# Performance work log

Measured on AMD Instinct MI355X. Metric: run time of the kernel, lower is better.

The kernel has to match this reference:

```python
import jax, jax.numpy as jnp
import numpy as np

B, H1, W1, C = 16, 32, 32, 256
H2, W2, C2 = 16, 16, 512
H3, W3, C3 = 8, 8, 1024
N1, N2, N3 = H1 * W1, H2 * W2, H3 * W3


def resize_bilinear_legacy(x, out_size):
    """Legacy tf.image.resize_images BILINEAR (align_corners=False,
    half_pixel_centers=False): src = dst * in/out. x: [B, H, W]."""
    def lerp_axis(a, in_size, axis):
        src = jnp.arange(out_size, dtype=jnp.float32) * (in_size / out_size)
        lo = jnp.floor(src).astype(jnp.int32)
        hi = jnp.minimum(lo + 1, in_size - 1)
        fr = (src - lo.astype(jnp.float32))
        shape = [1, 1, 1]
        shape[axis] = out_size
        fr = fr.reshape(shape)
        a_lo = jnp.take(a, lo, axis=axis)
        a_hi = jnp.take(a, hi, axis=axis)
        return a_lo * (1.0 - fr) + a_hi * fr

    x = lerp_axis(x, x.shape[1], axis=1)
    x = lerp_axis(x, x.shape[2], axis=2)
    return x


def setup_inputs() -> dict:
    key = jax.random.key(0)
    ks = jax.random.split(key, 10)
    s = lambda c: 1.0 / np.sqrt(c)
    return {
        "f1": jax.random.normal(ks[0], (B, H1, W1, C), jnp.float32),
        "f2": jax.random.normal(ks[1], (B, H2, W2, C2), jnp.float32),
        "f3": jax.random.normal(ks[2], (B, H3, W3, C3), jnp.float32),
        "w1": jax.random.normal(ks[3], (C, C), jnp.float32) * s(C),
        "b1": jnp.zeros((C,), jnp.float32),
        "w2": jax.random.normal(ks[4], (C2, C), jnp.float32) * s(C2),
        "b2": jnp.zeros((C,), jnp.float32),
        "w3": jax.random.normal(ks[5], (C3, C), jnp.float32) * s(C3),
        "b3": jnp.zeros((C,), jnp.float32),
        # Keras 'uniform' init: U(-0.05, 0.05), shape (1,)
        "a1": jax.random.uniform(ks[6], (1,), jnp.float32, -0.05, 0.05),
        "a2": jax.random.uniform(ks[7], (1,), jnp.float32, -0.05, 0.05),
        "a3": jax.random.uniform(ks[8], (1,), jnp.float32, -0.05, 0.05),
    }


def reference(f1, f2, f3, w1, b1, w2, b2, w3, b3, a1, a2, a3):
    # 1x1 conv projections to C channels
    p1 = jnp.einsum("bhwc,cd->bhwd", f1, w1) + b1          # [B,H1,W1,C]
    p2 = jnp.einsum("bhwc,cd->bhwd", f2, w2) + b2          # [B,H2,W2,C]
    p3 = jnp.einsum("bhwc,cd->bhwd", f3, w3) + b3          # [B,H3,W3,C]

    x1 = p1.reshape(B, N1, C)
    x2 = p2.reshape(B, N2, C)
    x3 = p3.reshape(B, N3, C)

    att1 = jnp.einsum("bnc,bmc->bnm", x1, x1)              # [B,N1,N1]
    att2 = jnp.einsum("bnc,bmc->bnm", x2, x2)              # [B,N2,N2]
    att3 = jnp.einsum("bnc,bmc->bnm", x3, x3)              # [B,N3,N3]

    att2 = resize_bilinear_legacy(att2, N1)                # [B,N1,N1]
    att3 = resize_bilinear_legacy(att3, N1)                # [B,N1,N1]

    att = jax.nn.sigmoid(a1[0] * att1 + a2[0] * att2 + a3[0] * att3)

    out = jnp.einsum("bnm,bmc->bnc", att, x1)              # [B,N1,C]
    return p1 + out.reshape(B, H1, W1, C)
```

## Files before the change

### kernel.cpp

```cpp
#include <hip/hip_runtime.h>

typedef unsigned short ushort_t;
typedef short s16x8 __attribute__((ext_vector_type(8)));
typedef float f32x4 __attribute__((ext_vector_type(4)));

#define MFMA16(a, b, c) __builtin_amdgcn_mfma_f32_16x16x32_bf16((a), (b), (c), 0, 0, 0)

#define BATCH 16
#define N1 1024
#define C1 256
#define N2 256
#define N3 64
#define PB3 64
#define PB2 256
#define PB1 256
#define TSTRIDE 72

static __device__ __forceinline__ ushort_t f2b(float f) {
    unsigned int u = __builtin_bit_cast(unsigned int, f);
    unsigned int r = (u + 0x7fffu + ((u >> 16) & 1u)) >> 16;
    return (ushort_t)r;
}
static __device__ __forceinline__ float b2f(ushort_t b) {
    unsigned int u = ((unsigned int)b) << 16;
    return __builtin_bit_cast(float, u);
}

static __device__ __forceinline__ s16x8 cvt8(const float* p) {
    f32x4 lo = *reinterpret_cast<const f32x4*>(p);
    f32x4 hi = *reinterpret_cast<const f32x4*>(p + 4);
    s16x8 r;
#pragma unroll
    for (int i = 0; i < 4; ++i) {
        r[i]     = (short)f2b(lo[i]);
        r[i + 4] = (short)f2b(hi[i]);
    }
    return r;
}

__global__ void k_wt(const float* __restrict__ w1, const float* __restrict__ w2,
                     const float* __restrict__ w3,
                     ushort_t* __restrict__ w1t, ushort_t* __restrict__ w2t,
                     ushort_t* __restrict__ w3t) {
    int i = blockIdx.x * 256 + threadIdx.x;
    if (i < 65536) {
        int d = i >> 8, k = i & 255;
        w1t[i] = f2b(w1[k * 256 + d]);
    } else if (i < 65536 + 131072) {
        int j = i - 65536;
        int d = j >> 9, k = j & 511;
        w2t[j] = f2b(w2[k * 256 + d]);
    } else if (i < 65536 + 131072 + 262144) {
        int j = i - 65536 - 131072;
        int d = j >> 10, k = j & 1023;
        w3t[j] = f2b(w3[k * 256 + d]);
    }
}

__global__ __launch_bounds__(256) void k_proj(
    const float* __restrict__ f1, const float* __restrict__ f2,
    const float* __restrict__ f3,
    const ushort_t* __restrict__ w1t, const ushort_t* __restrict__ w2t,
    const ushort_t* __restrict__ w3t,
    const float* __restrict__ b1, const float* __restrict__ b2,
    const float* __restrict__ b3,
    ushort_t* __restrict__ x1b, ushort_t* __restrict__ x1t,
    ushort_t* __restrict__ x2b, ushort_t* __restrict__ x3b)
{
    __shared__ ushort_t sT[256 * TSTRIDE];

    int bid = blockIdx.x;
    int w = threadIdx.x >> 6, l = threadIdx.x & 63;
    int lr = l & 15, lk = (l >> 4) * 8;

    if (bid < PB3 + PB2) {
        const float* A; const ushort_t* wt; const float* bias; ushort_t* xb; int K, tile;
        if (bid < PB3) { A = f3; wt = w3t; bias = b3; xb = x3b; K = 1024; tile = bid; }
        else           { A = f2; wt = w2t; bias = b2; xb = x2b; K = 512;  tile = bid - PB3; }
        int rowBase = tile * 16;

        const float* arow = A + (size_t)(rowBase + lr) * K + lk;
        f32x4 acc[4] = {};
        for (int kk = 0; kk < K; kk += 32) {
            s16x8 af = cvt8(arow + kk);
#pragma unroll
            for (int t = 0; t < 4; ++t) {
                const ushort_t* bp = wt + (size_t)(w * 64 + t * 16 + lr) * K + kk + lk;
                acc[t] = MFMA16(af, *reinterpret_cast<const s16x8*>(bp), acc[t]);
            }
        }
        int r0 = rowBase + (l >> 4) * 4;
#pragma unroll
        for (int t = 0; t < 4; ++t) {
            int c = w * 64 + t * 16 + lr;
            float bs = bias[c];
#pragma unroll
            for (int j = 0; j < 4; ++j) {
                float v = acc[t][j] + bs;
                xb[(size_t)(r0 + j) * 256 + c] = f2b(v);
            }
        }
    } else {
        int tile = bid - PB3 - PB2;
        int rowBase = tile * 64;
        const float* arow = f1 + (size_t)(rowBase + w * 16 + lr) * 256 + lk;

        f32x4 acc[16] = {};
        for (int kk = 0; kk < 256; kk += 32) {
            s16x8 af = cvt8(arow + kk);
#pragma unroll
            for (int t = 0; t < 16; ++t) {
                const ushort_t* bp = w1t + (size_t)(t * 16 + lr) * 256 + kk + lk;
                acc[t] = MFMA16(af, *reinterpret_cast<const s16x8*>(bp), acc[t]);
            }
        }
        int rl0 = w * 16 + (l >> 4) * 4;
        int r0 = rowBase + rl0;
#pragma unroll
        for (int t = 0; t < 16; ++t) {
            int c = t * 16 + lr;
            float bs = b1[c];
#pragma unroll
            for (int j = 0; j < 4; ++j) {
                float v = acc[t][j] + bs;
                ushort_t bits = f2b(v);
                x1b[(size_t)(r0 + j) * 256 + c] = bits;
                sT[c * TSTRIDE + rl0 + j] = bits;
            }
        }
        __syncthreads();
        int b = rowBase >> 10;
        int mBase = rowBase & 1023;
        int q = threadIdx.x & 3;
#pragma unroll
        for (int it = 0; it < 4; ++it) {
            int c = it * 64 + (threadIdx.x >> 2);
            const uint4* src = reinterpret_cast<const uint4*>(&sT[c * TSTRIDE + q * 16]);
            uint4* dst = reinterpret_cast<uint4*>(&x1t[((size_t)b * 256 + c) * 1024 + mBase + q * 16]);
            dst[0] = src[0];
            dst[1] = src[1];
        }
    }
}

__global__ __launch_bounds__(256) void k_xxt(
    const ushort_t* __restrict__ x2b, const ushort_t* __restrict__ x3b,
    float* __restrict__ att2, float* __restrict__ att3)
{
    int bid = blockIdx.x;
    const ushort_t* x; float* att; int n, b, bx, by;
    if (bid < 16) { x = x3b; att = att3; n = 64; b = bid; bx = 0; by = 0; }
    else {
        int j = bid - 16;
        x = x2b; att = att2; n = 256;
        b = j >> 4; bx = (j & 15) & 3; by = (j & 15) >> 2;
    }
    int w = threadIdx.x >> 6, l = threadIdx.x & 63;
    int lr = l & 15, lk = (l >> 4) * 8;
    int rowBase = bx * 64 + (w >> 1) * 32;
    int colBase = by * 64 + (w & 1) * 32;
    const ushort_t* xb = x + (size_t)b * n * 256;

    f32x4 acc[2][2] = {};
    for (int kk = 0; kk < 256; kk += 32) {
        s16x8 a[2], bb[2];
#pragma unroll
        for (int i = 0; i < 2; ++i)
            a[i] = *reinterpret_cast<const s16x8*>(xb + (size_t)(rowBase + i * 16 + lr) * 256 + kk + lk);
#pragma unroll
        for (int j = 0; j < 2; ++j)
            bb[j] = *reinterpret_cast<const s16x8*>(xb + (size_t)(colBase + j * 16 + lr) * 256 + kk + lk);
#pragma unroll
        for (int i = 0; i < 2; ++i)
#pragma unroll
            for (int j = 0; j < 2; ++j)
                acc[i][j] = MFMA16(a[i], bb[j], acc[i][j]);
    }
    float* ab = att + (size_t)b * n * n;
#pragma unroll
    for (int i = 0; i < 2; ++i)
#pragma unroll
        for (int j = 0; j < 2; ++j)
#pragma unroll
            for (int q = 0; q < 4; ++q) {
                int r = rowBase + i * 16 + (l >> 4) * 4 + q;
                int c = colBase + j * 16 + lr;
                ab[(size_t)r * n + c] = acc[i][j][q];
            }
}

__global__ __launch_bounds__(256) void k_att(
    const ushort_t* __restrict__ x1b, const float* __restrict__ att2,
    const float* __restrict__ att3,
    const float* __restrict__ a1p, const float* __restrict__ a2p, const float* __restrict__ a3p,
    ushort_t* __restrict__ att)
{
    int b = blockIdx.z;
    int w = threadIdx.x >> 6, l = threadIdx.x & 63;
    int lr = l & 15, lk = (l >> 4) * 8;
    int rowBase = blockIdx.x * 128 + (w >> 1) * 64;
    int colBase = blockIdx.y * 128 + (w & 1) * 64;
    const ushort_t* xb = x1b + (size_t)b * N1 * C1;

    f32x4 acc[4][4] = {};
    for (int kk = 0; kk < 256; kk += 32) {
        s16x8 a[4], bb[4];
#pragma unroll
        for (int i = 0; i < 4; ++i)
            a[i] = *reinterpret_cast<const s16x8*>(xb + (size_t)(rowBase + i * 16 + lr) * 256 + kk + lk);
#pragma unroll
        for (int j = 0; j < 4; ++j)
            bb[j] = *reinterpret_cast<const s16x8*>(xb + (size_t)(colBase + j * 16 + lr) * 256 + kk + lk);
#pragma unroll
        for (int i = 0; i < 4; ++i)
#pragma unroll
            for (int j = 0; j < 4; ++j)
                acc[i][j] = MFMA16(a[i], bb[j], acc[i][j]);
    }

    float a1 = *a1p, a2 = *a2p, a3 = *a3p;
    const float* A2 = att2 + (size_t)b * N2 * N2;
    const float* A3 = att3 + (size_t)b * N3 * N3;
    ushort_t* ab = att + (size_t)b * N1 * N1;

#pragma unroll
    for (int i = 0; i < 4; ++i)
#pragma unroll
        for (int j = 0; j < 4; ++j)
#pragma unroll
            for (int q = 0; q < 4; ++q) {
                int nn = rowBase + i * 16 + (l >> 4) * 4 + q;
                int mm = colBase + j * 16 + lr;
                int r2l = nn >> 2, c2l = mm >> 2;
                int r2h = min(r2l + 1, N2 - 1), c2h = min(c2l + 1, N2 - 1);
                float fr2 = (float)(nn & 3) * 0.25f, fc2 = (float)(mm & 3) * 0.25f;
                float v2 =
                    (1.f - fr2) * ((1.f - fc2) * A2[r2l * N2 + c2l] + fc2 * A2[r2l * N2 + c2h]) +
                    fr2 * ((1.f - fc2) * A2[r2h * N2 + c2l] + fc2 * A2[r2h * N2 + c2h]);
                int r3l = nn >> 4, c3l = mm >> 4;
                int r3h = min(r3l + 1, N3 - 1), c3h = min(c3l + 1, N3 - 1);
                float fr3 = (float)(nn & 15) * 0.0625f, fc3 = (float)(mm & 15) * 0.0625f;
                float v3 =
                    (1.f - fr3) * ((1.f - fc3) * A3[r3l * N3 + c3l] + fc3 * A3[r3l * N3 + c3h]) +
                    fr3 * ((1.f - fc3) * A3[r3h * N3 + c3l] + fc3 * A3[r3h * N3 + c3h]);
                float s = a1 * acc[i][j][q] + a2 * v2 + a3 * v3;
                float sig = 1.f / (1.f + __expf(-s));
                ab[(size_t)nn * N1 + mm] = f2b(sig);
            }
}

__global__ __launch_bounds__(256) void k_pv(
    const ushort_t* __restrict__ att, const ushort_t* __restrict__ x1t,
    const ushort_t* __restrict__ x1b, float* __restrict__ out)
{
    int b = blockIdx.z;
    int w = threadIdx.x >> 6, l = threadIdx.x & 63;
    int lr = l & 15, lk = (l >> 4) * 8;
    int rowBase = blockIdx.x * 128 + (w >> 1) * 64;
    int colBase = blockIdx.y * 128 + (w & 1) * 64;
    const ushort_t* ab = att + (size_t)b * N1 * N1;
    const ushort_t* xt = x1t + (size_t)b * C1 * N1;

    f32x4 acc[4][4] = {};
    for (int kk = 0; kk < 1024; kk += 32) {
        s16x8 a[4], bb[4];
#pragma unroll
        for (int i = 0; i < 4; ++i)
            a[i] = *reinterpret_cast<const s16x8*>(ab + (size_t)(rowBase + i * 16 + lr) * N1 + kk + lk);
#pragma unroll
        for (int j = 0; j < 4; ++j)
            bb[j] = *reinterpret_cast<const s16x8*>(xt + (size_t)(colBase + j * 16 + lr) * N1 + kk + lk);
#pragma unroll
        for (int i = 0; i < 4; ++i)
#pragma unroll
            for (int j = 0; j < 4; ++j)
                acc[i][j] = MFMA16(a[i], bb[j], acc[i][j]);
    }
#pragma unroll
    for (int i = 0; i < 4; ++i)
#pragma unroll
        for (int j = 0; j < 4; ++j)
#pragma unroll
            for (int q = 0; q < 4; ++q) {
                int r = rowBase + i * 16 + (l >> 4) * 4 + q;
                int c = colBase + j * 16 + lr;
                size_t idx = ((size_t)b * N1 + r) * C1 + c;
                out[idx] = b2f(x1b[idx]) + acc[i][j][q];
            }
}

extern "C" void kernel_launch(void* const* d_in, const int* in_sizes, int n_in,
                              void* d_out, int out_size, void* d_ws, size_t ws_size,
                              hipStream_t stream) {
    const float* f1 = (const float*)d_in[0];
    const float* f2 = (const float*)d_in[1];
    const float* f3 = (const float*)d_in[2];
    const float* w1 = (const float*)d_in[3];
    const float* b1 = (const float*)d_in[4];
    const float* w2 = (const float*)d_in[5];
    const float* b2 = (const float*)d_in[6];
    const float* w3 = (const float*)d_in[7];
    const float* b3 = (const float*)d_in[8];
    const float* a1 = (const float*)d_in[9];
    const float* a2 = (const float*)d_in[10];
    const float* a3 = (const float*)d_in[11];

    char* ws = (char*)d_ws;
    size_t off = 0;
    auto alloc = [&](size_t bytes) -> void* {
        void* p = ws + off;
        off += (bytes + 255) & ~(size_t)255;
        return p;
    };
    ushort_t* w1t = (ushort_t*)alloc((size_t)256 * 256 * 2);
    ushort_t* w2t = (ushort_t*)alloc((size_t)256 * 512 * 2);
    ushort_t* w3t = (ushort_t*)alloc((size_t)256 * 1024 * 2);
    ushort_t* x1b = (ushort_t*)alloc((size_t)BATCH * N1 * C1 * 2);
    ushort_t* x1t = (ushort_t*)alloc((size_t)BATCH * N1 * C1 * 2);
    ushort_t* x2b = (ushort_t*)alloc((size_t)BATCH * N2 * C1 * 2);
    ushort_t* x3b = (ushort_t*)alloc((size_t)BATCH * N3 * C1 * 2);
    float*    att2 = (float*)alloc((size_t)BATCH * N2 * N2 * 4);
    float*    att3 = (float*)alloc((size_t)BATCH * N3 * N3 * 4);
    ushort_t* attb = (ushort_t*)alloc((size_t)BATCH * N1 * N1 * 2);

    k_wt<<<(65536 + 131072 + 262144 + 255) / 256, 256, 0, stream>>>(w1, w2, w3, w1t, w2t, w3t);

    k_proj<<<PB3 + PB2 + PB1, 256, 0, stream>>>(f1, f2, f3, w1t, w2t, w3t,
                                                b1, b2, b3, x1b, x1t, x2b, x3b);

    k_xxt<<<16 + 256, 256, 0, stream>>>(x2b, x3b, att2, att3);

    k_att<<<dim3(N1 / 128, N1 / 128, BATCH), 256, 0, stream>>>(x1b, att2, att3, a1, a2, a3, attb);

    k_pv<<<dim3(N1 / 128, C1 / 128, BATCH), 256, 0, stream>>>(attb, x1t, x1b, (float*)d_out);
}
```

Baseline: 247.0 us.

## Fuse attention score, sigmoid and PV into flash-style kernel without materialized matrix

Merges the attention-score kernel and the P·V kernel into one streaming kernel. Each wave keeps 16 query rows in registers, computes 16x32 score tiles, applies bilinear-resized att2/att3 and the sigmoid, reshuffles the tile into A-operand layout with lane shuffles, and accumulates against V. This avoids writing and re-reading the 16x1024x1024 bf16 attention matrix. The trade-off is a grid of only 256 blocks with no LDS reuse, so every wave reloads keys and V from cache. The projection of f1 is also retiled to 32-row blocks with a smaller transpose buffer, and a few loops get unroll pragmas.

```diff
diff --git a/kernel.cpp b/kernel.cpp
--- a/kernel.cpp
+++ b/kernel.cpp
@@ -13,8 +13,8 @@
 #define N3 64
 #define PB3 64
 #define PB2 256
-#define PB1 256
-#define TSTRIDE 72
+#define PB1 512
+#define TST 40
 
 static __device__ __forceinline__ ushort_t f2b(float f) {
     unsigned int u = __builtin_bit_cast(unsigned int, f);
@@ -57,6 +57,35 @@
     }
 }
 
+template <int K>
+static __device__ __forceinline__ void proj16(
+    const float* __restrict__ A, const ushort_t* __restrict__ wt,
+    const float* __restrict__ bias, ushort_t* __restrict__ xb,
+    int tile, int w, int lr, int lk)
+{
+    int rowBase = tile * 16;
+    const float* arow = A + (size_t)(rowBase + lr) * K + lk;
+    f32x4 acc[4] = {};
+#pragma unroll 4
+    for (int kk = 0; kk < K; kk += 32) {
+        s16x8 af = cvt8(arow + kk);
+#pragma unroll
+        for (int t = 0; t < 4; ++t) {
+            const ushort_t* bp = wt + (size_t)(w * 64 + t * 16 + lr) * K + kk + lk;
+            acc[t] = MFMA16(af, *reinterpret_cast<const s16x8*>(bp), acc[t]);
+        }
+    }
+    int r0 = rowBase + (lk >> 3) * 4;
+#pragma unroll
+    for (int t = 0; t < 4; ++t) {
+        int c = w * 64 + t * 16 + lr;
+        float bs = bias[c];
+#pragma unroll
+        for (int j = 0; j < 4; ++j)
+            xb[(size_t)(r0 + j) * 256 + c] = f2b(acc[t][j] + bs);
+    }
+}
+
 __global__ __launch_bounds__(256) void k_proj(
     const float* __restrict__ f1, const float* __restrict__ f2,
     const float* __restrict__ f3,
@@ -67,79 +96,52 @@
     ushort_t* __restrict__ x1b, ushort_t* __restrict__ x1t,
     ushort_t* __restrict__ x2b, ushort_t* __restrict__ x3b)
 {
-    __shared__ ushort_t sT[256 * TSTRIDE];
+    __shared__ ushort_t sT[256 * TST];
 
     int bid = blockIdx.x;
     int w = threadIdx.x >> 6, l = threadIdx.x & 63;
-    int lr = l & 15, lk = (l >> 4) * 8;
-
-    if (bid < PB3 + PB2) {
-        const float* A; const ushort_t* wt; const float* bias; ushort_t* xb; int K, tile;
-        if (bid < PB3) { A = f3; wt = w3t; bias = b3; xb = x3b; K = 1024; tile = bid; }
-        else           { A = f2; wt = w2t; bias = b2; xb = x2b; K = 512;  tile = bid - PB3; }
-        int rowBase = tile * 16;
-
-        const float* arow = A + (size_t)(rowBase + lr) * K + lk;
-        f32x4 acc[4] = {};
-        for (int kk = 0; kk < K; kk += 32) {
+    int lr = l & 15, g = l >> 4, lk = g * 8;
+
+    if (bid < PB3) {
+        proj16<1024>(f3, w3t, b3, x3b, bid, w, lr, lk);
+    } else if (bid < PB3 + PB2) {
+        proj16<512>(f2, w2t, b2, x2b, bid - PB3, w, lr, lk);
+    } else {
+        int tile = bid - PB3 - PB2;
+        int rowBase = tile * 32;
+        int rowHalf = w & 1, colHalf = w >> 1;
+        const float* arow = f1 + (size_t)(rowBase + rowHalf * 16 + lr) * 256 + lk;
+
+        f32x4 acc[8] = {};
+#pragma unroll 2
+        for (int kk = 0; kk < 256; kk += 32) {
             s16x8 af = cvt8(arow + kk);
 #pragma unroll
-            for (int t = 0; t < 4; ++t) {
-                const ushort_t* bp = wt + (size_t)(w * 64 + t * 16 + lr) * K + kk + lk;
+            for (int t = 0; t < 8; ++t) {
+                const ushort_t* bp = w1t + (size_t)(colHalf * 128 + t * 16 + lr) * 256 + kk + lk;
                 acc[t] = MFMA16(af, *reinterpret_cast<const s16x8*>(bp), acc[t]);
             }
         }
-        int r0 = rowBase + (l >> 4) * 4;
-#pragma unroll
-        for (int t = 0; t < 4; ++t) {
-            int c = w * 64 + t * 16 + lr;
-            float bs = bias[c];
-#pragma unroll
-            for (int j = 0; j < 4; ++j) {
-                float v = acc[t][j] + bs;
-                xb[(size_t)(r0 + j) * 256 + c] = f2b(v);
-            }
-        }
-    } else {
-        int tile = bid - PB3 - PB2;
-        int rowBase = tile * 64;
-        const float* arow = f1 + (size_t)(rowBase + w * 16 + lr) * 256 + lk;
-
-        f32x4 acc[16] = {};
-        for (int kk = 0; kk < 256; kk += 32) {
-            s16x8 af = cvt8(arow + kk);
-#pragma unroll
-            for (int t = 0; t < 16; ++t) {
-                const ushort_t* bp = w1t + (size_t)(t * 16 + lr) * 256 + kk + lk;
-                acc[t] = MFMA16(af, *reinterpret_cast<const s16x8*>(bp), acc[t]);
-            }
-        }
-        int rl0 = w * 16 + (l >> 4) * 4;
-        int r0 = rowBase + rl0;
-#pragma unroll
-        for (int t = 0; t < 16; ++t) {
-            int c = t * 16 + lr;
+        int rl0 = rowHalf * 16 + g * 4;
+#pragma unroll
+        for (int t = 0; t < 8; ++t) {
+            int c = colHalf * 128 + t * 16 + lr;
             float bs = b1[c];
 #pragma unroll
             for (int j = 0; j < 4; ++j) {
                 float v = acc[t][j] + bs;
                 ushort_t bits = f2b(v);
-                x1b[(size_t)(r0 + j) * 256 + c] = bits;
-                sT[c * TSTRIDE + rl0 + j] = bits;
+                x1b[(size_t)(rowBase + rl0 + j) * 256 + c] = bits;
+                sT[c * TST + rl0 + j] = bits;
             }
         }
         __syncthreads();
-        int b = rowBase >> 10;
-        int mBase = rowBase & 1023;
-        int q = threadIdx.x & 3;
-#pragma unroll
-        for (int it = 0; it < 4; ++it) {
-            int c = it * 64 + (threadIdx.x >> 2);
-            const uint4* src = reinterpret_cast<const uint4*>(&sT[c * TSTRIDE + q * 16]);
-            uint4* dst = reinterpret_cast<uint4*>(&x1t[((size_t)b * 256 + c) * 1024 + mBase + q * 16]);
-            dst[0] = src[0];
-            dst[1] = src[1];
-        }
+        int b = rowBase >> 10, mBase = rowBase & 1023;
+        int c = threadIdx.x;
+        const uint4* src = reinterpret_cast<const uint4*>(&sT[c * TST]);
+        uint4* dst = reinterpret_cast<uint4*>(&x1t[(((size_t)b * 256 + c) << 10) + mBase]);
+#pragma unroll
+        for (int q = 0; q < 4; ++q) dst[q] = src[q];
     }
 }
 
@@ -162,6 +164,7 @@
     const ushort_t* xb = x + (size_t)b * n * 256;
 
     f32x4 acc[2][2] = {};
+#pragma unroll 2
     for (int kk = 0; kk < 256; kk += 32) {
         s16x8 a[2], bb[2];
 #pragma unroll
@@ -189,104 +192,98 @@
             }
 }
 
-__global__ __launch_bounds__(256) void k_att(
-    const ushort_t* __restrict__ x1b, const float* __restrict__ att2,
-    const float* __restrict__ att3,
-    const float* __restrict__ a1p, const float* __restrict__ a2p, const float* __restrict__ a3p,
-    ushort_t* __restrict__ att)
+__global__ __launch_bounds__(256) void k_attpv(
+    const ushort_t* __restrict__ x1b, const ushort_t* __restrict__ x1t,
+    const float* __restrict__ att2, const float* __restrict__ att3,
+    const float* __restrict__ a1p, const float* __restrict__ a2p,
+    const float* __restrict__ a3p, float* __restrict__ out)
 {
-    int b = blockIdx.z;
+    int b = blockIdx.y;
     int w = threadIdx.x >> 6, l = threadIdx.x & 63;
-    int lr = l & 15, lk = (l >> 4) * 8;
-    int rowBase = blockIdx.x * 128 + (w >> 1) * 64;
-    int colBase = blockIdx.y * 128 + (w & 1) * 64;
-    const ushort_t* xb = x1b + (size_t)b * N1 * C1;
-
-    f32x4 acc[4][4] = {};
-    for (int kk = 0; kk < 256; kk += 32) {
-        s16x8 a[4], bb[4];
-#pragma unroll
-        for (int i = 0; i < 4; ++i)
-            a[i] = *reinterpret_cast<const s16x8*>(xb + (size_t)(rowBase + i * 16 + lr) * 256 + kk + lk);
-#pragma unroll
-        for (int j = 0; j < 4; ++j)
-            bb[j] = *reinterpret_cast<const s16x8*>(xb + (size_t)(colBase + j * 16 + lr) * 256 + kk + lk);
-#pragma unroll
-        for (int i = 0; i < 4; ++i)
-#pragma unroll
-            for (int j = 0; j < 4; ++j)
-                acc[i][j] = MFMA16(a[i], bb[j], acc[i][j]);
-    }
-
-    float a1 = *a1p, a2 = *a2p, a3 = *a3p;
+    int idx = l & 15, g = l >> 4;
+    int rowBase = blockIdx.x * 64 + w * 16;
+    const ushort_t* X = x1b + (size_t)b * N1 * C1;
+    const ushort_t* V = x1t + (size_t)b * C1 * N1;
+
+    s16x8 rf[8];
+    const ushort_t* rowp = X + (size_t)(rowBase + idx) * 256 + g * 8;
+#pragma unroll
+    for (int ks = 0; ks < 8; ++ks) rf[ks] = *reinterpret_cast<const s16x8*>(rowp + ks * 32);
+
+    int nn = rowBase + idx;
     const float* A2 = att2 + (size_t)b * N2 * N2;
     const float* A3 = att3 + (size_t)b * N3 * N3;
-    ushort_t* ab = att + (size_t)b * N1 * N1;
-
-#pragma unroll
-    for (int i = 0; i < 4; ++i)
-#pragma unroll
-        for (int j = 0; j < 4; ++j)
-#pragma unroll
-            for (int q = 0; q < 4; ++q) {
-                int nn = rowBase + i * 16 + (l >> 4) * 4 + q;
-                int mm = colBase + j * 16 + lr;
-                int r2l = nn >> 2, c2l = mm >> 2;
-                int r2h = min(r2l + 1, N2 - 1), c2h = min(c2l + 1, N2 - 1);
-                float fr2 = (float)(nn & 3) * 0.25f, fc2 = (float)(mm & 3) * 0.25f;
-                float v2 =
-                    (1.f - fr2) * ((1.f - fc2) * A2[r2l * N2 + c2l] + fc2 * A2[r2l * N2 + c2h]) +
-                    fr2 * ((1.f - fc2) * A2[r2h * N2 + c2l] + fc2 * A2[r2h * N2 + c2h]);
-                int r3l = nn >> 4, c3l = mm >> 4;
-                int r3h = min(r3l + 1, N3 - 1), c3h = min(c3l + 1, N3 - 1);
-                float fr3 = (float)(nn & 15) * 0.0625f, fc3 = (float)(mm & 15) * 0.0625f;
-                float v3 =
-                    (1.f - fr3) * ((1.f - fc3) * A3[r3l * N3 + c3l] + fc3 * A3[r3l * N3 + c3h]) +
-                    fr3 * ((1.f - fc3) * A3[r3h * N3 + c3l] + fc3 * A3[r3h * N3 + c3h]);
-                float s = a1 * acc[i][j][q] + a2 * v2 + a3 * v3;
-                float sig = 1.f / (1.f + __expf(-s));
-                ab[(size_t)nn * N1 + mm] = f2b(sig);
-            }
-}
-
-__global__ __launch_bounds__(256) void k_pv(
-    const ushort_t* __restrict__ att, const ushort_t* __restrict__ x1t,
-    const ushort_t* __restrict__ x1b, float* __restrict__ out)
-{
-    int b = blockIdx.z;
-    int w = threadIdx.x >> 6, l = threadIdx.x & 63;
-    int lr = l & 15, lk = (l >> 4) * 8;
-    int rowBase = blockIdx.x * 128 + (w >> 1) * 64;
-    int colBase = blockIdx.y * 128 + (w & 1) * 64;
-    const ushort_t* ab = att + (size_t)b * N1 * N1;
-    const ushort_t* xt = x1t + (size_t)b * C1 * N1;
-
-    f32x4 acc[4][4] = {};
-    for (int kk = 0; kk < 1024; kk += 32) {
-        s16x8 a[4], bb[4];
-#pragma unroll
-        for (int i = 0; i < 4; ++i)
-            a[i] = *reinterpret_cast<const s16x8*>(ab + (size_t)(rowBase + i * 16 + lr) * N1 + kk + lk);
-#pragma unroll
-        for (int j = 0; j < 4; ++j)
-            bb[j] = *reinterpret_cast<const s16x8*>(xt + (size_t)(colBase + j * 16 + lr) * N1 + kk + lk);
-#pragma unroll
-        for (int i = 0; i < 4; ++i)
-#pragma unroll
-            for (int j = 0; j < 4; ++j)
-                acc[i][j] = MFMA16(a[i], bb[j], acc[i][j]);
-    }
-#pragma unroll
-    for (int i = 0; i < 4; ++i)
-#pragma unroll
-        for (int j = 0; j < 4; ++j)
-#pragma unroll
-            for (int q = 0; q < 4; ++q) {
-                int r = rowBase + i * 16 + (l >> 4) * 4 + q;
-                int c = colBase + j * 16 + lr;
-                size_t idx = ((size_t)b * N1 + r) * C1 + c;
-                out[idx] = b2f(x1b[idx]) + acc[i][j][q];
-            }
+    int r2l = nn >> 2; int r2h = min(r2l + 1, N2 - 1); float fr2 = (float)(nn & 3) * 0.25f;
+    const float* A2lo = A2 + r2l * N2; const float* A2hi = A2 + r2h * N2;
+    int r3l = nn >> 4; int r3h = min(r3l + 1, N3 - 1); float fr3 = (float)(nn & 15) * 0.0625f;
+    const float* A3lo = A3 + r3l * N3; const float* A3hi = A3 + r3h * N3;
+    float a1 = *a1p, a2 = *a2p, a3 = *a3p;
+
+    f32x4 acc[16] = {};
+
+    for (int mm0 = 0; mm0 < N1; mm0 += 32) {
+        f32x4 t0 = {}, t1 = {};
+        const ushort_t* c0 = X + (size_t)(mm0 + idx) * 256 + g * 8;
+        const ushort_t* c1 = c0 + 16 * 256;
+#pragma unroll
+        for (int ks = 0; ks < 8; ++ks) {
+            s16x8 ca = *reinterpret_cast<const s16x8*>(c0 + ks * 32);
+            s16x8 cb = *reinterpret_cast<const s16x8*>(c1 + ks * 32);
+            t0 = MFMA16(ca, rf[ks], t0);
+            t1 = MFMA16(cb, rf[ks], t1);
+        }
+        int c2a = (mm0 >> 2) + g;        int c2ah = min(c2a + 1, N2 - 1);
+        int c2b = ((mm0 + 16) >> 2) + g; int c2bh = min(c2b + 1, N2 - 1);
+        float p00 = A2lo[c2a], p01 = A2lo[c2ah], p10 = A2hi[c2a], p11 = A2hi[c2ah];
+        float q00 = A2lo[c2b], q01 = A2lo[c2bh], q10 = A2hi[c2b], q11 = A2hi[c2bh];
+        int c3a = mm0 >> 4; int c3ah = min(c3a + 1, N3 - 1); int c3bh = min(c3a + 2, N3 - 1);
+        float s00 = A3lo[c3a], s01 = A3lo[c3ah], s10 = A3hi[c3a], s11 = A3hi[c3ah];
+        float u01 = A3lo[c3bh], u11 = A3hi[c3bh];
+#pragma unroll
+        for (int r = 0; r < 4; ++r) {
+            float fc2 = (float)r * 0.25f;
+            float fc3 = (float)(g * 4 + r) * 0.0625f;
+            float e0 = p00 + fc2 * (p01 - p00), e1 = p10 + fc2 * (p11 - p10);
+            float v2 = e0 + fr2 * (e1 - e0);
+            float f0 = s00 + fc3 * (s01 - s00), f1v = s10 + fc3 * (s11 - s10);
+            float v3 = f0 + fr3 * (f1v - f0);
+            float s = a1 * t0[r] + a2 * v2 + a3 * v3;
+            t0[r] = 1.f / (1.f + __expf(-s));
+            e0 = q00 + fc2 * (q01 - q00); e1 = q10 + fc2 * (q11 - q10);
+            v2 = e0 + fr2 * (e1 - e0);
+            f0 = s01 + fc3 * (u01 - s01); f1v = s11 + fc3 * (u11 - s11);
+            v3 = f0 + fr3 * (f1v - f0);
+            s = a1 * t1[r] + a2 * v2 + a3 * v3;
+            t1[r] = 1.f / (1.f + __expf(-s));
+        }
+        int base0 = ((2 * g) & 3) * 16 + idx;
+        int base1 = ((2 * g + 1) & 3) * 16 + idx;
+        bool hi = g >= 2;
+        s16x8 pa;
+#pragma unroll
+        for (int r = 0; r < 4; ++r) {
+            float v00 = __shfl(t0[r], base0); float v10 = __shfl(t1[r], base0);
+            float v01 = __shfl(t0[r], base1); float v11 = __shfl(t1[r], base1);
+            pa[r]     = (short)f2b(hi ? v10 : v00);
+            pa[4 + r] = (short)f2b(hi ? v11 : v01);
+        }
+        const ushort_t* vp = V + (size_t)idx * N1 + mm0 + g * 8;
+#pragma unroll
+        for (int cf = 0; cf < 16; ++cf) {
+            s16x8 bv = *reinterpret_cast<const s16x8*>(vp + (size_t)cf * 16 * N1);
+            acc[cf] = MFMA16(pa, bv, acc[cf]);
+        }
+    }
+#pragma unroll
+    for (int cf = 0; cf < 16; ++cf) {
+#pragma unroll
+        for (int q = 0; q < 4; ++q) {
+            int r = rowBase + g * 4 + q;
+            int c = cf * 16 + idx;
+            size_t o = ((size_t)b * N1 + r) * C1 + c;
+            out[o] = b2f(X[(size_t)r * 256 + c]) + acc[cf][q];
+        }
+    }
 }
 
 extern "C" void kernel_launch(void* const* d_in, const int* in_sizes, int n_in,
@@ -321,7 +318,6 @@
     ushort_t* x3b = (ushort_t*)alloc((size_t)BATCH * N3 * C1 * 2);
     float*    att2 = (float*)alloc((size_t)BATCH * N2 * N2 * 4);
     float*    att3 = (float*)alloc((size_t)BATCH * N3 * N3 * 4);
-    ushort_t* attb = (ushort_t*)alloc((size_t)BATCH * N1 * N1 * 2);
 
     k_wt<<<(65536 + 131072 + 262144 + 255) / 256, 256, 0, stream>>>(w1, w2, w3, w1t, w2t, w3t);
 
@@ -330,7 +326,6 @@
 
     k_xxt<<<16 + 256, 256, 0, stream>>>(x2b, x3b, att2, att3);
 
-    k_att<<<dim3(N1 / 128, N1 / 128, BATCH), 256, 0, stream>>>(x1b, att2, att3, a1, a2, a3, attb);
-
-    k_pv<<<dim3(N1 / 128, C1 / 128, BATCH), 256, 0, stream>>>(attb, x1t, x1b, (float*)d_out);
-}
+    k_attpv<<<dim3(16, BATCH), 256, 0, stream>>>(x1b, x1t, att2, att3,
+                                                 a1, a2, a3, (float*)d_out);
+}
```

After: 279.6 us. 13.2% more time.

## Stage GEMM tiles through double-buffered LDS with async global-to-LDS loads

Applied to the files above, without the earlier changes.

The attention-score and PV GEMM kernels now copy their A/B tiles into double-buffered shared memory with global_load_lds instead of each wave loading MFMA fragments directly from global memory. This gives more reuse and overlaps the next tile's load with the current MFMAs. The grids are flattened with a batch-interleaved block order, and k_pv moves to 512 threads with a 64-wide K step. The projection kernel is split into a templated helper and transposes x1 in two halves to cut LDS use, with some loops partially unrolled. The cost is more LDS per block and a barrier every K step.

```diff
diff --git a/kernel.cpp b/kernel.cpp
--- a/kernel.cpp
+++ b/kernel.cpp
@@ -14,7 +14,7 @@
 #define PB3 64
 #define PB2 256
 #define PB1 256
-#define TSTRIDE 72
+#define TST 72
 
 static __device__ __forceinline__ ushort_t f2b(float f) {
     unsigned int u = __builtin_bit_cast(unsigned int, f);
@@ -25,7 +25,6 @@
     unsigned int u = ((unsigned int)b) << 16;
     return __builtin_bit_cast(float, u);
 }
-
 static __device__ __forceinline__ s16x8 cvt8(const float* p) {
     f32x4 lo = *reinterpret_cast<const f32x4*>(p);
     f32x4 hi = *reinterpret_cast<const f32x4*>(p + 4);
@@ -36,6 +35,28 @@
         r[i + 4] = (short)f2b(hi[i]);
     }
     return r;
+}
+
+template <int BK, int NW>
+static __device__ __forceinline__ void stage_tile(
+    const ushort_t* __restrict__ g, int rowBase, int rowStride, int kOff,
+    ushort_t* lds, int w, int l)
+{
+    constexpr int SEGS = (128 * BK) / 512;
+    constexpr int PW   = SEGS / NW;
+    constexpr int LPR  = BK / 8;
+    constexpr int RPS  = 512 / BK;
+#pragma unroll
+    for (int c = 0; c < PW; ++c) {
+        int seg = w * PW + c;
+        int row = seg * RPS + l / LPR;
+        int col = (l % LPR) * 8;
+        const ushort_t* src = g + (size_t)(rowBase + row) * rowStride + kOff + col;
+        __builtin_amdgcn_global_load_lds(
+            (const __attribute__((address_space(1))) unsigned int*)src,
+            (__attribute__((address_space(3))) unsigned int*)(lds + seg * 512),
+            16, 0, 0);
+    }
 }
 
 __global__ void k_wt(const float* __restrict__ w1, const float* __restrict__ w2,
@@ -57,6 +78,35 @@
     }
 }
 
+template <int K>
+static __device__ __forceinline__ void proj16(
+    const float* __restrict__ A, const ushort_t* __restrict__ wt,
+    const float* __restrict__ bias, ushort_t* __restrict__ xb,
+    int tile, int w, int lr, int lk)
+{
+    int rowBase = tile * 16;
+    const float* arow = A + (size_t)(rowBase + lr) * K + lk;
+    f32x4 acc[4] = {};
+#pragma unroll 4
+    for (int kk = 0; kk < K; kk += 32) {
+        s16x8 af = cvt8(arow + kk);
+#pragma unroll
+        for (int t = 0; t < 4; ++t) {
+            const ushort_t* bp = wt + (size_t)(w * 64 + t * 16 + lr) * K + kk + lk;
+            acc[t] = MFMA16(af, *reinterpret_cast<const s16x8*>(bp), acc[t]);
+        }
+    }
+    int r0 = rowBase + (lk >> 3) * 4;
+#pragma unroll
+    for (int t = 0; t < 4; ++t) {
+        int c = w * 64 + t * 16 + lr;
+        float bs = bias[c];
+#pragma unroll
+        for (int j = 0; j < 4; ++j)
+            xb[(size_t)(r0 + j) * 256 + c] = f2b(acc[t][j] + bs);
+    }
+}
+
 __global__ __launch_bounds__(256) void k_proj(
     const float* __restrict__ f1, const float* __restrict__ f2,
     const float* __restrict__ f3,
@@ -67,45 +117,22 @@
     ushort_t* __restrict__ x1b, ushort_t* __restrict__ x1t,
     ushort_t* __restrict__ x2b, ushort_t* __restrict__ x3b)
 {
-    __shared__ ushort_t sT[256 * TSTRIDE];
+    __shared__ ushort_t sT[128 * TST];
 
     int bid = blockIdx.x;
     int w = threadIdx.x >> 6, l = threadIdx.x & 63;
-    int lr = l & 15, lk = (l >> 4) * 8;
-
-    if (bid < PB3 + PB2) {
-        const float* A; const ushort_t* wt; const float* bias; ushort_t* xb; int K, tile;
-        if (bid < PB3) { A = f3; wt = w3t; bias = b3; xb = x3b; K = 1024; tile = bid; }
-        else           { A = f2; wt = w2t; bias = b2; xb = x2b; K = 512;  tile = bid - PB3; }
-        int rowBase = tile * 16;
-
-        const float* arow = A + (size_t)(rowBase + lr) * K + lk;
-        f32x4 acc[4] = {};
-        for (int kk = 0; kk < K; kk += 32) {
-            s16x8 af = cvt8(arow + kk);
-#pragma unroll
-            for (int t = 0; t < 4; ++t) {
-                const ushort_t* bp = wt + (size_t)(w * 64 + t * 16 + lr) * K + kk + lk;
-                acc[t] = MFMA16(af, *reinterpret_cast<const s16x8*>(bp), acc[t]);
-            }
-        }
-        int r0 = rowBase + (l >> 4) * 4;
-#pragma unroll
-        for (int t = 0; t < 4; ++t) {
-            int c = w * 64 + t * 16 + lr;
-            float bs = bias[c];
-#pragma unroll
-            for (int j = 0; j < 4; ++j) {
-                float v = acc[t][j] + bs;
-                xb[(size_t)(r0 + j) * 256 + c] = f2b(v);
-            }
-        }
+    int lr = l & 15, g = l >> 4, lk = g * 8;
+
+    if (bid < PB3) {
+        proj16<1024>(f3, w3t, b3, x3b, bid, w, lr, lk);
+    } else if (bid < PB3 + PB2) {
+        proj16<512>(f2, w2t, b2, x2b, bid - PB3, w, lr, lk);
     } else {
         int tile = bid - PB3 - PB2;
         int rowBase = tile * 64;
         const float* arow = f1 + (size_t)(rowBase + w * 16 + lr) * 256 + lk;
-
         f32x4 acc[16] = {};
+#pragma unroll 2
         for (int kk = 0; kk < 256; kk += 32) {
             s16x8 af = cvt8(arow + kk);
 #pragma unroll
@@ -114,31 +141,30 @@
                 acc[t] = MFMA16(af, *reinterpret_cast<const s16x8*>(bp), acc[t]);
             }
         }
-        int rl0 = w * 16 + (l >> 4) * 4;
-        int r0 = rowBase + rl0;
-#pragma unroll
-        for (int t = 0; t < 16; ++t) {
-            int c = t * 16 + lr;
-            float bs = b1[c];
-#pragma unroll
-            for (int j = 0; j < 4; ++j) {
-                float v = acc[t][j] + bs;
-                ushort_t bits = f2b(v);
-                x1b[(size_t)(r0 + j) * 256 + c] = bits;
-                sT[c * TSTRIDE + rl0 + j] = bits;
+        int rl0 = w * 16 + g * 4;
+        int bIdx = rowBase >> 10, mBase = rowBase & 1023;
+#pragma unroll
+        for (int p = 0; p < 2; ++p) {
+            if (p) __syncthreads();
+#pragma unroll
+            for (int t = 0; t < 8; ++t) {
+                int tt = p * 8 + t;
+                int c = tt * 16 + lr;
+                float bs = b1[c];
+#pragma unroll
+                for (int j = 0; j < 4; ++j) {
+                    float v = acc[tt][j] + bs;
+                    ushort_t bits = f2b(v);
+                    x1b[(size_t)(rowBase + rl0 + j) * 256 + c] = bits;
+                    sT[(c - p * 128) * TST + rl0 + j] = bits;
+                }
             }
-        }
-        __syncthreads();
-        int b = rowBase >> 10;
-        int mBase = rowBase & 1023;
-        int q = threadIdx.x & 3;
-#pragma unroll
-        for (int it = 0; it < 4; ++it) {
-            int c = it * 64 + (threadIdx.x >> 2);
-            const uint4* src = reinterpret_cast<const uint4*>(&sT[c * TSTRIDE + q * 16]);
-            uint4* dst = reinterpret_cast<uint4*>(&x1t[((size_t)b * 256 + c) * 1024 + mBase + q * 16]);
-            dst[0] = src[0];
-            dst[1] = src[1];
+            __syncthreads();
+            int cl = threadIdx.x >> 1, q = threadIdx.x & 1;
+            const uint4* src = reinterpret_cast<const uint4*>(&sT[cl * TST + q * 32]);
+            uint4* dst = reinterpret_cast<uint4*>(
+                &x1t[(((size_t)bIdx * 256 + p * 128 + cl) << 10) + mBase + q * 32]);
+            dst[0] = src[0]; dst[1] = src[1]; dst[2] = src[2]; dst[3] = src[3];
         }
     }
 }
@@ -162,6 +188,7 @@
     const ushort_t* xb = x + (size_t)b * n * 256;
 
     f32x4 acc[2][2] = {};
+#pragma unroll 2
     for (int kk = 0; kk < 256; kk += 32) {
         s16x8 a[2], bb[2];
 #pragma unroll
@@ -190,47 +217,65 @@
 }
 
 __global__ __launch_bounds__(256) void k_att(
-    const ushort_t* __restrict__ x1b, const float* __restrict__ att2,
-    const float* __restrict__ att3,
-    const float* __restrict__ a1p, const float* __restrict__ a2p, const float* __restrict__ a3p,
-    ushort_t* __restrict__ att)
-{
-    int b = blockIdx.z;
+    const ushort_t* __restrict__ x1b,
+    const float* __restrict__ att2, const float* __restrict__ att3,
+    const float* __restrict__ a1p, const float* __restrict__ a2p,
+    const float* __restrict__ a3p, ushort_t* __restrict__ att)
+{
+    __shared__ ushort_t As[2][128 * 32];
+    __shared__ ushort_t Bs[2][128 * 32];
+
+    int i = blockIdx.x;
+    int b = (i & 7) | ((i >> 9) << 3);
+    int tile = (i >> 3) & 63;
+    int rowT = (tile >> 3) * 128, colT = (tile & 7) * 128;
+
     int w = threadIdx.x >> 6, l = threadIdx.x & 63;
-    int lr = l & 15, lk = (l >> 4) * 8;
-    int rowBase = blockIdx.x * 128 + (w >> 1) * 64;
-    int colBase = blockIdx.y * 128 + (w & 1) * 64;
-    const ushort_t* xb = x1b + (size_t)b * N1 * C1;
+    int idx = l & 15, g = l >> 4;
+    int rowHalf = w >> 1, colHalf = w & 1;
+
+    const ushort_t* X = x1b + (size_t)b * N1 * C1;
+
+    stage_tile<32, 4>(X, rowT, 256, 0, As[0], w, l);
+    stage_tile<32, 4>(X, colT, 256, 0, Bs[0], w, l);
 
     f32x4 acc[4][4] = {};
-    for (int kk = 0; kk < 256; kk += 32) {
-        s16x8 a[4], bb[4];
-#pragma unroll
-        for (int i = 0; i < 4; ++i)
-            a[i] = *reinterpret_cast<const s16x8*>(xb + (size_t)(rowBase + i * 16 + lr) * 256 + kk + lk);
-#pragma unroll
-        for (int j = 0; j < 4; ++j)
-            bb[j] = *reinterpret_cast<const s16x8*>(xb + (size_t)(colBase + j * 16 + lr) * 256 + kk + lk);
-#pragma unroll
-        for (int i = 0; i < 4; ++i)
-#pragma unroll
-            for (int j = 0; j < 4; ++j)
-                acc[i][j] = MFMA16(a[i], bb[j], acc[i][j]);
+    for (int t = 0; t < 8; ++t) {
+        __syncthreads();
+        if (t < 7) {
+            stage_tile<32, 4>(X, rowT, 256, (t + 1) * 32, As[(t + 1) & 1], w, l);
+            stage_tile<32, 4>(X, colT, 256, (t + 1) * 32, Bs[(t + 1) & 1], w, l);
+        }
+        const ushort_t* Ab = As[t & 1];
+        const ushort_t* Bb = Bs[t & 1];
+        s16x8 af[4], bf[4];
+#pragma unroll
+        for (int ii = 0; ii < 4; ++ii)
+            af[ii] = *reinterpret_cast<const s16x8*>(Ab + (rowHalf * 64 + ii * 16 + idx) * 32 + g * 8);
+#pragma unroll
+        for (int jj = 0; jj < 4; ++jj)
+            bf[jj] = *reinterpret_cast<const s16x8*>(Bb + (colHalf * 64 + jj * 16 + idx) * 32 + g * 8);
+#pragma unroll
+        for (int ii = 0; ii < 4; ++ii)
+#pragma unroll
+            for (int jj = 0; jj < 4; ++jj)
+                acc[ii][jj] = MFMA16(af[ii], bf[jj], acc[ii][jj]);
     }
 
     float a1 = *a1p, a2 = *a2p, a3 = *a3p;
     const float* A2 = att2 + (size_t)b * N2 * N2;
     const float* A3 = att3 + (size_t)b * N3 * N3;
     ushort_t* ab = att + (size_t)b * N1 * N1;
-
-#pragma unroll
-    for (int i = 0; i < 4; ++i)
-#pragma unroll
-        for (int j = 0; j < 4; ++j)
+    int rowW = rowT + rowHalf * 64, colW = colT + colHalf * 64;
+
+#pragma unroll
+    for (int ii = 0; ii < 4; ++ii)
+#pragma unroll
+        for (int jj = 0; jj < 4; ++jj)
 #pragma unroll
             for (int q = 0; q < 4; ++q) {
-                int nn = rowBase + i * 16 + (l >> 4) * 4 + q;
-                int mm = colBase + j * 16 + lr;
+                int nn = rowW + ii * 16 + g * 4 + q;
+                int mm = colW + jj * 16 + idx;
                 int r2l = nn >> 2, c2l = mm >> 2;
                 int r2h = min(r2l + 1, N2 - 1), c2h = min(c2l + 1, N2 - 1);
                 float fr2 = (float)(nn & 3) * 0.25f, fc2 = (float)(mm & 3) * 0.25f;
@@ -243,49 +288,71 @@
                 float v3 =
                     (1.f - fr3) * ((1.f - fc3) * A3[r3l * N3 + c3l] + fc3 * A3[r3l * N3 + c3h]) +
                     fr3 * ((1.f - fc3) * A3[r3h * N3 + c3l] + fc3 * A3[r3h * N3 + c3h]);
-                float s = a1 * acc[i][j][q] + a2 * v2 + a3 * v3;
+                float s = a1 * acc[ii][jj][q] + a2 * v2 + a3 * v3;
                 float sig = 1.f / (1.f + __expf(-s));
                 ab[(size_t)nn * N1 + mm] = f2b(sig);
             }
 }
 
-__global__ __launch_bounds__(256) void k_pv(
+__global__ __launch_bounds__(512) void k_pv(
     const ushort_t* __restrict__ att, const ushort_t* __restrict__ x1t,
     const ushort_t* __restrict__ x1b, float* __restrict__ out)
 {
-    int b = blockIdx.z;
+    __shared__ ushort_t As[2][128 * 64];
+    __shared__ ushort_t Bs[2][128 * 64];
+
+    int i = blockIdx.x;
+    int b = (i & 7) | (((i >> 7) & 1) << 3);
+    int tile = (i >> 3) & 15;
+    int rowT = (tile & 7) * 128, colT = (tile >> 3) * 128;
+
     int w = threadIdx.x >> 6, l = threadIdx.x & 63;
-    int lr = l & 15, lk = (l >> 4) * 8;
-    int rowBase = blockIdx.x * 128 + (w >> 1) * 64;
-    int colBase = blockIdx.y * 128 + (w & 1) * 64;
-    const ushort_t* ab = att + (size_t)b * N1 * N1;
-    const ushort_t* xt = x1t + (size_t)b * C1 * N1;
-
-    f32x4 acc[4][4] = {};
-    for (int kk = 0; kk < 1024; kk += 32) {
-        s16x8 a[4], bb[4];
-#pragma unroll
-        for (int i = 0; i < 4; ++i)
-            a[i] = *reinterpret_cast<const s16x8*>(ab + (size_t)(rowBase + i * 16 + lr) * N1 + kk + lk);
-#pragma unroll
-        for (int j = 0; j < 4; ++j)
-            bb[j] = *reinterpret_cast<const s16x8*>(xt + (size_t)(colBase + j * 16 + lr) * N1 + kk + lk);
-#pragma unroll
-        for (int i = 0; i < 4; ++i)
-#pragma unroll
-            for (int j = 0; j < 4; ++j)
-                acc[i][j] = MFMA16(a[i], bb[j], acc[i][j]);
-    }
-#pragma unroll
-    for (int i = 0; i < 4; ++i)
-#pragma unroll
-        for (int j = 0; j < 4; ++j)
+    int idx = l & 15, g = l >> 4;
+    int rowHalf = w >> 2;
+    int colQ = w & 3;
+
+    const ushort_t* A = att + (size_t)b * N1 * N1;
+    const ushort_t* B = x1t + (size_t)b * C1 * N1;
+
+    stage_tile<64, 8>(A, rowT, 1024, 0, As[0], w, l);
+    stage_tile<64, 8>(B, colT, 1024, 0, Bs[0], w, l);
+
+    f32x4 acc[4][2] = {};
+    for (int t = 0; t < 16; ++t) {
+        __syncthreads();
+        if (t < 15) {
+            stage_tile<64, 8>(A, rowT, 1024, (t + 1) * 64, As[(t + 1) & 1], w, l);
+            stage_tile<64, 8>(B, colT, 1024, (t + 1) * 64, Bs[(t + 1) & 1], w, l);
+        }
+        const ushort_t* Ab = As[t & 1];
+        const ushort_t* Bb = Bs[t & 1];
+#pragma unroll
+        for (int kk = 0; kk < 64; kk += 32) {
+            s16x8 af[4], bf[2];
+#pragma unroll
+            for (int ii = 0; ii < 4; ++ii)
+                af[ii] = *reinterpret_cast<const s16x8*>(Ab + (rowHalf * 64 + ii * 16 + idx) * 64 + kk + g * 8);
+#pragma unroll
+            for (int jj = 0; jj < 2; ++jj)
+                bf[jj] = *reinterpret_cast<const s16x8*>(Bb + (colQ * 32 + jj * 16 + idx) * 64 + kk + g * 8);
+#pragma unroll
+            for (int ii = 0; ii < 4; ++ii)
+#pragma unroll
+                for (int jj = 0; jj < 2; ++jj)
+                    acc[ii][jj] = MFMA16(af[ii], bf[jj], acc[ii][jj]);
+        }
+    }
+    int rowW = rowT + rowHalf * 64, colW = colT + colQ * 32;
+#pragma unroll
+    for (int ii = 0; ii < 4; ++ii)
+#pragma unroll
+        for (int jj = 0; jj < 2; ++jj)
 #pragma unroll
             for (int q = 0; q < 4; ++q) {
-                int r = rowBase + i * 16 + (l >> 4) * 4 + q;
-                int c = colBase + j * 16 + lr;
-                size_t idx = ((size_t)b * N1 + r) * C1 + c;
-                out[idx] = b2f(x1b[idx]) + acc[i][j][q];
+                int r = rowW + ii * 16 + g * 4 + q;
+                int c = colW + jj * 16 + idx;
+                size_t o = ((size_t)b * N1 + r) * C1 + c;
+                out[o] = b2f(x1b[(size_t)b * N1 * C1 + (size_t)r * 256 + c]) + acc[ii][jj][q];
             }
 }
 
@@ -330,7 +397,7 @@
 
     k_xxt<<<16 + 256, 256, 0, stream>>>(x2b, x3b, att2, att3);
 
-    k_att<<<dim3(N1 / 128, N1 / 128, BATCH), 256, 0, stream>>>(x1b, att2, att3, a1, a2, a3, attb);
-
-    k_pv<<<dim3(N1 / 128, C1 / 128, BATCH), 256, 0, stream>>>(attb, x1t, x1b, (float*)d_out);
-}
+    k_att<<<1024, 256, 0, stream>>>(x1b, att2, att3, a1, a2, a3, attb);
+
+    k_pv<<<256, 512, 0, stream>>>(attb, x1t, x1b, (float*)d_out);
+}
```

Result: faster. 213.8 us (-13.4%).
